# Optimization experiments

Measured on AMD Instinct MI355X. Metric: run time of the kernel, lower is better.

Reference implementation:

```python
import jax, jax.numpy as jnp
import numpy as np

# Hough voting constants from the call site:
# Hough(angle=90, R2_list=[4,64,256,1024], num_classes=1, region_num=13, vote_field_size=33)
ANGLE = 90
R2_LIST = (4, 64, 256, 1024)
REGION_NUM = 13
VFS = 33  # vote field size


def _hough_filter():
    """Log-polar vote-field filter [region_num, VFS, VFS].

    Region 0 = center disk (r^2 <= R2_LIST[0]); region 1 + ring*4 + angle_bin
    for the 3 radius rings x 4 angle sectors. Each region's weights are
    1/(#pixels in region) so each region's vote sums to 1 (HoughNet log map).
    """
    c = VFS // 2
    ys, xs = np.meshgrid(np.arange(VFS) - c, np.arange(VFS) - c, indexing='ij')
    r2 = xs ** 2 + ys ** 2
    theta = (np.degrees(np.arctan2(ys, xs)) + 360.0) % 360.0
    nang = 360 // ANGLE  # 4 angle sectors
    abin = np.minimum((theta // ANGLE).astype(np.int64), nang - 1)
    region = -np.ones((VFS, VFS), np.int64)
    region[r2 <= R2_LIST[0]] = 0
    for i in range(1, len(R2_LIST)):
        m = (r2 > R2_LIST[i - 1]) & (r2 <= R2_LIST[i])
        region[m] = 1 + (i - 1) * nang + abin[m]
    filt = np.zeros((REGION_NUM, VFS, VFS), np.float32)
    for r in range(REGION_NUM):
        m = region == r
        if m.sum() > 0:
            filt[r][m] = 1.0 / float(m.sum())
    return filt


# ConvTranspose2d(13 -> 1, k=33, stride=1, pad=16) == SAME conv with flipped kernel.
_HOUGH_CONV_W = jnp.asarray(np.flip(_hough_filter(), axis=(1, 2))[None].copy())  # [1,13,33,33]


def setup_inputs() -> dict:
    key = jax.random.key(0)
    ks = jax.random.split(key, 4)
    B, C, H, W = 2, 256, 256, 512
    return {
        'x': jax.random.normal(ks[0], (B, C, H, W), jnp.float32),
        'pos_w': jax.random.normal(ks[1], (13, C), jnp.float32) * 0.05,
        'pos_b': jnp.zeros((13,), jnp.float32),
        'reg_w': jax.random.normal(ks[2], (1, C), jnp.float32) * 0.05,
        'reg_b': jnp.zeros((1,), jnp.float32),
        'off_w': jax.random.normal(ks[3], (2, C), jnp.float32) * 0.05,
        'off_b': jnp.zeros((2,), jnp.float32),
    }


def _conv1x1(x, w, b):
    # x: [B,C,H,W], w: [O,C] -> [B,O,H,W]
    return jnp.einsum('bchw,oc->bohw', x, w) + b[None, :, None, None]


def reference(x, pos_w, pos_b, reg_w, reg_b, off_w, off_b):
    evident = jax.nn.relu(_conv1x1(x, pos_w, pos_b))  # [B,13,H,W]
    score = jax.lax.conv_general_dilated(
        evident, _HOUGH_CONV_W, (1, 1), 'SAME',
        dimension_numbers=('NCHW', 'OIHW', 'NCHW'))  # [B,1,H,W]
    x_cls = jax.nn.sigmoid(score)
    x_reg = _conv1x1(x, reg_w, reg_b)
    x_off = _conv1x1(x, off_w, off_b)
    return (x_cls, x_reg, x_off)
```

## Files before the change

### kernel.cpp

```cpp
#include <hip/hip_runtime.h>
#include <math.h>

#define BB   2
#define CC   256
#define HH   256
#define WW   512
#define HW   (HH*WW)
#define IMG  (CC*HW)

#define HPP  288
#define WPP  546
#define CHPP (HPP*WPP)
#define EVB2 (13*CHPP)
#define EV2_FLOATS (BB*EVB2)

#define OUT_REG (BB*HW)
#define OUT_OFF (2*BB*HW)

static __device__ __forceinline__ int region_of(int ys, int xs) {
    int r2 = ys * ys + xs * xs;
    int bin;
    if (ys == 0)     bin = (xs >= 0) ? 0 : 2;
    else if (ys > 0) bin = (xs > 0) ? 0 : 1;
    else             bin = (xs < 0) ? 2 : 3;
    if (r2 <= 4)   return 0;
    if (r2 <= 64)  return 1 + bin;
    if (r2 <= 256) return 5 + bin;
    return 9 + bin;
}

__global__ void repack_w(const float* __restrict__ pw, const float* __restrict__ pb,
                         const float* __restrict__ rw, const float* __restrict__ rb,
                         const float* __restrict__ ow, const float* __restrict__ ob,
                         float* __restrict__ wp, float* __restrict__ bias) {
    int i = blockIdx.x * blockDim.x + threadIdx.x;
    if (i < 4096) {
        int c = i >> 4, o = i & 15;
        float v;
        if (o < 13)       v = pw[o * CC + c];
        else if (o == 13) v = rw[c];
        else              v = ow[(o - 14) * CC + c];
        wp[c * 16 + o] = v;
    }
    if (i < 16) {
        float v = (i < 13) ? pb[i] : (i == 13 ? rb[0] : ob[i - 14]);
        bias[i] = v;
    }
}

__global__ __launch_bounds__(256) void conv1x1_k(
    const float* __restrict__ x, const float* __restrict__ wp,
    const float* __restrict__ bias, float* __restrict__ ev,
    float* __restrict__ out) {
    __shared__ float4 wlds[1024];
    int tid = threadIdx.x;
    const float4* wp4 = (const float4*)wp;
#pragma unroll
    for (int j = 0; j < 4; j++) wlds[tid + j * 256] = wp4[tid + j * 256];
    __syncthreads();

    int g  = blockIdx.x * 256 + tid;
    int b  = g >> 17;
    int hw = g & (HW - 1);
    const float* xb = x + (size_t)b * IMG + hw;

    float acc[16];
#pragma unroll
    for (int o = 0; o < 16; o++) acc[o] = 0.f;

#pragma unroll 4
    for (int c = 0; c < CC; c++) {
        float v = xb[c * HW];
        float4 w[4];
#pragma unroll
        for (int j = 0; j < 4; j++) w[j] = wlds[c * 4 + j];
        const float* wf = (const float*)w;
#pragma unroll
        for (int o = 0; o < 16; o++) acc[o] = fmaf(v, wf[o], acc[o]);
    }

    int y0 = hw >> 9, x0 = hw & 511;
    float* evb = ev + (size_t)b * EVB2 + (y0 + 16) * WPP + (x0 + 18);
#pragma unroll
    for (int o = 0; o < 13; o++) {
        evb[o * CHPP] = fmaxf(acc[o] + bias[o], 0.f);
    }
    out[OUT_REG + b * HW + hw] = acc[13] + bias[13];
    out[OUT_OFF + b * 2 * HW + hw]      = acc[14] + bias[14];
    out[OUT_OFF + b * 2 * HW + HW + hw] = acc[15] + bias[15];
}

__global__ __launch_bounds__(256) void prefix_k(float* __restrict__ ev) {
    int row  = blockIdx.x * 4 + (threadIdx.x >> 6);
    int lane = threadIdx.x & 63;
    if (row >= BB * 13 * HPP) return;
    float* r = ev + (size_t)row * WPP;
    float carry = 0.f;
    for (int seg = 0; seg < WPP; seg += 64) {
        int i = seg + lane;
        float v = (i < WPP) ? r[i] : 0.f;
#pragma unroll
        for (int d = 1; d < 64; d <<= 1) {
            float t = __shfl_up(v, d, 64);
            if (lane >= d) v += t;
        }
        v += carry;
        if (i < WPP) r[i] = v;
        carry = __shfl(v, 63, 64);
    }
}

__global__ __launch_bounds__(256) void hough_k(const float* __restrict__ P,
                                               float* __restrict__ out) {
    __shared__ int  cnt[13];
    __shared__ int  runbuf[33 * 16];
    __shared__ int  countrow[33];
    __shared__ int  rowstart[34];
    __shared__ int2 tab[608];
    int tid = threadIdx.x;
    if (tid < 13) cnt[tid] = 0;
    __syncthreads();

    for (int i = tid; i < 1089; i += 256) {
        int ky = i / 33, kx = i - ky * 33;
        atomicAdd(&cnt[region_of(16 - ky, 16 - kx)], 1);
    }
    __syncthreads();

    if (tid < 33) {
        int ky = tid, n = 0;
        int c0 = region_of(16 - ky, 16);
        int kxa = 0;
        for (int kx = 1; kx <= 33; kx++) {
            int c = (kx < 33) ? region_of(16 - ky, 16 - kx) : -1;
            if (c != c0) {
                runbuf[tid * 16 + n] = c0 | (kxa << 4) | ((kx - 1) << 10);
                n++;
                c0 = c; kxa = kx;
            }
        }
        countrow[tid] = n;
    }
    __syncthreads();

    if (tid == 0) {
        int a = 0;
        for (int t = 0; t < 33; t++) { rowstart[t] = a; a += countrow[t]; }
        rowstart[33] = a;
    }
    __syncthreads();

    if (tid < 33) {
        int ky = tid, base = rowstart[tid], n = countrow[tid];
        for (int j = 0; j < n; j++) {
            int rn  = runbuf[tid * 16 + j];
            int c   = rn & 15, kxa = (rn >> 4) & 63, kxb = (rn >> 10) & 63;
            float w = 1.0f / (float)cnt[c];
            int off0 = c * CHPP + (ky - 16) * WPP;
            tab[2 * (base + j)]     = make_int2(off0 + (kxb - 16), __float_as_int(w));
            tab[2 * (base + j) + 1] = make_int2(off0 + (kxa - 17), __float_as_int(-w));
        }
    }
    __syncthreads();
    int m = 2 * rowstart[33];

    int bid = blockIdx.x;
    int sb  = (bid & 7) * 128 + (bid >> 3);
    int p   = sb * 256 + tid;
    int b   = p >> 17;
    int hw  = p & (HW - 1);
    int y   = hw >> 9, xx = hw & 511;
    const float* Pb = P + (size_t)b * EVB2 + (y + 16) * WPP + (xx + 18);

    float s = 0.f;
#pragma unroll 4
    for (int t = 0; t < m; t++) {
        int2 e = tab[t];
        s = fmaf(Pb[e.x], __int_as_float(e.y), s);
    }
    out[b * HW + hw] = 1.0f / (1.0f + expf(-s));
}

extern "C" void kernel_launch(void* const* d_in, const int* in_sizes, int n_in,
                              void* d_out, int out_size, void* d_ws, size_t ws_size,
                              hipStream_t stream) {
    const float* x  = (const float*)d_in[0];
    const float* pw = (const float*)d_in[1];
    const float* pb = (const float*)d_in[2];
    const float* rw = (const float*)d_in[3];
    const float* rb = (const float*)d_in[4];
    const float* ow = (const float*)d_in[5];
    const float* ob = (const float*)d_in[6];
    float* out = (float*)d_out;

    float* ev   = (float*)d_ws;
    float* wp   = ev + EV2_FLOATS;
    float* bias = wp + 4096;

    hipMemsetAsync(ev, 0, (size_t)EV2_FLOATS * sizeof(float), stream);
    repack_w<<<16, 256, 0, stream>>>(pw, pb, rw, rb, ow, ob, wp, bias);
    conv1x1_k<<<1024, 256, 0, stream>>>(x, wp, bias, ev, out);
    prefix_k<<<1872, 256, 0, stream>>>(ev);
    hough_k<<<1024, 256, 0, stream>>>(ev, out);
}
```

Before: 411.9 us.

## Precompute hough table once, vectorize conv1x1 over two pixels, skip padded prefix rows

```diff
diff --git a/kernel.cpp b/kernel.cpp
--- a/kernel.cpp
+++ b/kernel.cpp
@@ -29,22 +29,69 @@
     return 9 + bin;
 }
 
-__global__ void repack_w(const float* __restrict__ pw, const float* __restrict__ pb,
-                         const float* __restrict__ rw, const float* __restrict__ rb,
-                         const float* __restrict__ ow, const float* __restrict__ ob,
-                         float* __restrict__ wp, float* __restrict__ bias) {
-    int i = blockIdx.x * blockDim.x + threadIdx.x;
-    if (i < 4096) {
+__global__ void setup_k(const float* __restrict__ pw, const float* __restrict__ pb,
+                        const float* __restrict__ rw, const float* __restrict__ rb,
+                        const float* __restrict__ ow, const float* __restrict__ ob,
+                        float* __restrict__ wp, float* __restrict__ bias,
+                        int2* __restrict__ tabg, int* __restrict__ mg) {
+    int blk = blockIdx.x, tid = threadIdx.x;
+    if (blk < 16) {
+        int i = blk * 256 + tid;
         int c = i >> 4, o = i & 15;
         float v;
         if (o < 13)       v = pw[o * CC + c];
         else if (o == 13) v = rw[c];
         else              v = ow[(o - 14) * CC + c];
         wp[c * 16 + o] = v;
-    }
-    if (i < 16) {
-        float v = (i < 13) ? pb[i] : (i == 13 ? rb[0] : ob[i - 14]);
-        bias[i] = v;
+        if (i < 16) {
+            float bv = (i < 13) ? pb[i] : (i == 13 ? rb[0] : ob[i - 14]);
+            bias[i] = bv;
+        }
+    } else {
+        __shared__ int cnt[13];
+        __shared__ int runbuf[33 * 16];
+        __shared__ int countrow[33];
+        __shared__ int rowstart[34];
+        if (tid < 13) cnt[tid] = 0;
+        __syncthreads();
+        for (int i = tid; i < 1089; i += 256) {
+            int ky = i / 33, kx = i - ky * 33;
+            atomicAdd(&cnt[region_of(16 - ky, 16 - kx)], 1);
+        }
+        __syncthreads();
+        if (tid < 33) {
+            int ky = tid, n = 0;
+            int c0 = region_of(16 - ky, 16);
+            int kxa = 0;
+            for (int kx = 1; kx <= 33; kx++) {
+                int c = (kx < 33) ? region_of(16 - ky, 16 - kx) : -1;
+                if (c != c0) {
+                    runbuf[tid * 16 + n] = c0 | (kxa << 4) | ((kx - 1) << 10);
+                    n++;
+                    c0 = c; kxa = kx;
+                }
+            }
+            countrow[tid] = n;
+        }
+        __syncthreads();
+        if (tid == 0) {
+            int a = 0;
+            for (int t = 0; t < 33; t++) { rowstart[t] = a; a += countrow[t]; }
+            rowstart[33] = a;
+            mg[0] = 2 * a;
+        }
+        __syncthreads();
+        if (tid < 33) {
+            int ky = tid, base = rowstart[tid], n = countrow[tid];
+            for (int j = 0; j < n; j++) {
+                int rn  = runbuf[tid * 16 + j];
+                int c   = rn & 15, kxa = (rn >> 4) & 63, kxb = (rn >> 10) & 63;
+                float w = 1.0f / (float)cnt[c];
+                int off0 = c * CHPP + (ky - 16) * WPP;
+                tabg[2 * (base + j)]     = make_int2(off0 + (kxb - 16), __float_as_int(w));
+                tabg[2 * (base + j) + 1] = make_int2(off0 + (kxa - 17), __float_as_int(-w));
+            }
+        }
     }
 }
 
@@ -52,118 +99,77 @@
     const float* __restrict__ x, const float* __restrict__ wp,
     const float* __restrict__ bias, float* __restrict__ ev,
     float* __restrict__ out) {
-    __shared__ float4 wlds[1024];
     int tid = threadIdx.x;
-    const float4* wp4 = (const float4*)wp;
-#pragma unroll
-    for (int j = 0; j < 4; j++) wlds[tid + j * 256] = wp4[tid + j * 256];
-    __syncthreads();
-
     int g  = blockIdx.x * 256 + tid;
-    int b  = g >> 17;
-    int hw = g & (HW - 1);
+    int p  = g * 2;
+    int b  = p >> 17;
+    int hw = p & (HW - 1);
     const float* xb = x + (size_t)b * IMG + hw;
 
-    float acc[16];
-#pragma unroll
-    for (int o = 0; o < 16; o++) acc[o] = 0.f;
+    float acc0[16], acc1[16];
+#pragma unroll
+    for (int o = 0; o < 16; o++) { acc0[o] = 0.f; acc1[o] = 0.f; }
 
 #pragma unroll 4
     for (int c = 0; c < CC; c++) {
-        float v = xb[c * HW];
-        float4 w[4];
-#pragma unroll
-        for (int j = 0; j < 4; j++) w[j] = wlds[c * 4 + j];
-        const float* wf = (const float*)w;
-#pragma unroll
-        for (int o = 0; o < 16; o++) acc[o] = fmaf(v, wf[o], acc[o]);
+        float2 v = *(const float2*)(xb + c * HW);
+        const float* wr = wp + c * 16;
+#pragma unroll
+        for (int o = 0; o < 16; o++) {
+            float wv = wr[o];
+            acc0[o] = fmaf(v.x, wv, acc0[o]);
+            acc1[o] = fmaf(v.y, wv, acc1[o]);
+        }
     }
 
     int y0 = hw >> 9, x0 = hw & 511;
     float* evb = ev + (size_t)b * EVB2 + (y0 + 16) * WPP + (x0 + 18);
 #pragma unroll
     for (int o = 0; o < 13; o++) {
-        evb[o * CHPP] = fmaxf(acc[o] + bias[o], 0.f);
-    }
-    out[OUT_REG + b * HW + hw] = acc[13] + bias[13];
-    out[OUT_OFF + b * 2 * HW + hw]      = acc[14] + bias[14];
-    out[OUT_OFF + b * 2 * HW + HW + hw] = acc[15] + bias[15];
+        float bo = bias[o];
+        *(float2*)(evb + o * CHPP) =
+            make_float2(fmaxf(acc0[o] + bo, 0.f), fmaxf(acc1[o] + bo, 0.f));
+    }
+    float rbv = bias[13];
+    *(float2*)(out + OUT_REG + b * HW + hw) = make_float2(acc0[13] + rbv, acc1[13] + rbv);
+#pragma unroll
+    for (int o = 14; o < 16; o++) {
+        float bo = bias[o];
+        *(float2*)(out + OUT_OFF + b * 2 * HW + (o - 14) * HW + hw) =
+            make_float2(acc0[o] + bo, acc1[o] + bo);
+    }
 }
 
 __global__ __launch_bounds__(256) void prefix_k(float* __restrict__ ev) {
-    int row  = blockIdx.x * 4 + (threadIdx.x >> 6);
+    int r    = blockIdx.x * 4 + (threadIdx.x >> 6);
     int lane = threadIdx.x & 63;
-    if (row >= BB * 13 * HPP) return;
-    float* r = ev + (size_t)row * WPP;
+    if (r >= BB * 13 * HH) return;
+    int b   = r / (13 * HH);
+    int rem = r - b * (13 * HH);
+    int ch  = rem >> 8;
+    int y   = rem & 255;
+    float* row = ev + (size_t)(b * 13 + ch) * CHPP + (size_t)(y + 16) * WPP;
     float carry = 0.f;
     for (int seg = 0; seg < WPP; seg += 64) {
         int i = seg + lane;
-        float v = (i < WPP) ? r[i] : 0.f;
+        float v = (i < WPP) ? row[i] : 0.f;
 #pragma unroll
         for (int d = 1; d < 64; d <<= 1) {
             float t = __shfl_up(v, d, 64);
             if (lane >= d) v += t;
         }
         v += carry;
-        if (i < WPP) r[i] = v;
+        if (i < WPP) row[i] = v;
         carry = __shfl(v, 63, 64);
     }
 }
 
 __global__ __launch_bounds__(256) void hough_k(const float* __restrict__ P,
+                                               const int2* __restrict__ tabg,
+                                               const int* __restrict__ mg,
                                                float* __restrict__ out) {
-    __shared__ int  cnt[13];
-    __shared__ int  runbuf[33 * 16];
-    __shared__ int  countrow[33];
-    __shared__ int  rowstart[34];
-    __shared__ int2 tab[608];
+    int m   = mg[0];
     int tid = threadIdx.x;
-    if (tid < 13) cnt[tid] = 0;
-    __syncthreads();
-
-    for (int i = tid; i < 1089; i += 256) {
-        int ky = i / 33, kx = i - ky * 33;
-        atomicAdd(&cnt[region_of(16 - ky, 16 - kx)], 1);
-    }
-    __syncthreads();
-
-    if (tid < 33) {
-        int ky = tid, n = 0;
-        int c0 = region_of(16 - ky, 16);
-        int kxa = 0;
-        for (int kx = 1; kx <= 33; kx++) {
-            int c = (kx < 33) ? region_of(16 - ky, 16 - kx) : -1;
-            if (c != c0) {
-                runbuf[tid * 16 + n] = c0 | (kxa << 4) | ((kx - 1) << 10);
-                n++;
-                c0 = c; kxa = kx;
-            }
-        }
-        countrow[tid] = n;
-    }
-    __syncthreads();
-
-    if (tid == 0) {
-        int a = 0;
-        for (int t = 0; t < 33; t++) { rowstart[t] = a; a += countrow[t]; }
-        rowstart[33] = a;
-    }
-    __syncthreads();
-
-    if (tid < 33) {
-        int ky = tid, base = rowstart[tid], n = countrow[tid];
-        for (int j = 0; j < n; j++) {
-            int rn  = runbuf[tid * 16 + j];
-            int c   = rn & 15, kxa = (rn >> 4) & 63, kxb = (rn >> 10) & 63;
-            float w = 1.0f / (float)cnt[c];
-            int off0 = c * CHPP + (ky - 16) * WPP;
-            tab[2 * (base + j)]     = make_int2(off0 + (kxb - 16), __float_as_int(w));
-            tab[2 * (base + j) + 1] = make_int2(off0 + (kxa - 17), __float_as_int(-w));
-        }
-    }
-    __syncthreads();
-    int m = 2 * rowstart[33];
-
     int bid = blockIdx.x;
     int sb  = (bid & 7) * 128 + (bid >> 3);
     int p   = sb * 256 + tid;
@@ -173,9 +179,9 @@
     const float* Pb = P + (size_t)b * EVB2 + (y + 16) * WPP + (xx + 18);
 
     float s = 0.f;
-#pragma unroll 4
+#pragma unroll 8
     for (int t = 0; t < m; t++) {
-        int2 e = tab[t];
+        int2 e = tabg[t];
         s = fmaf(Pb[e.x], __int_as_float(e.y), s);
     }
     out[b * HW + hw] = 1.0f / (1.0f + expf(-s));
@@ -196,10 +202,12 @@
     float* ev   = (float*)d_ws;
     float* wp   = ev + EV2_FLOATS;
     float* bias = wp + 4096;
+    int2*  tabg = (int2*)(bias + 16);
+    int*   mg   = (int*)(tabg + 2048);
 
     hipMemsetAsync(ev, 0, (size_t)EV2_FLOATS * sizeof(float), stream);
-    repack_w<<<16, 256, 0, stream>>>(pw, pb, rw, rb, ow, ob, wp, bias);
-    conv1x1_k<<<1024, 256, 0, stream>>>(x, wp, bias, ev, out);
-    prefix_k<<<1872, 256, 0, stream>>>(ev);
-    hough_k<<<1024, 256, 0, stream>>>(ev, out);
-}
+    setup_k<<<17, 256, 0, stream>>>(pw, pb, rw, rb, ow, ob, wp, bias, tabg, mg);
+    conv1x1_k<<<512, 256, 0, stream>>>(x, wp, bias, ev, out);
+    prefix_k<<<1664, 256, 0, stream>>>(ev);
+    hough_k<<<1024, 256, 0, stream>>>(ev, tabg, mg, out);
+}
```

New measurement: 402.2 us. 1.02x faster.
